# Kernel tuning notes

Measured on AMD Instinct MI355X. Metric: run time of the kernel, lower is better.

Reference implementation:

```python
import jax
import jax.numpy as jnp
import numpy as np

EPSILON = 0.05
MAX_STEPS = 50
N0 = 2048
M0 = 2048


def setup_inputs() -> dict:
    key = jax.random.key(0)
    C = jax.random.uniform(key, (N0, M0), dtype=jnp.float32)
    return {"C": C}


def _sinkhorn(C):
    n0, m0 = C.shape
    # dummy=True: pad right by n0 cols, bottom by m0 rows with zeros -> square (n0+m0, m0+n0)
    C = jnp.pad(C, ((0, m0), (0, n0)), mode="constant", constant_values=0.0)
    n, m = C.shape
    logp = jnp.full((n,), -jnp.log(jnp.float32(n)), dtype=C.dtype)
    logq = jnp.full((m,), -jnp.log(jnp.float32(m)), dtype=C.dtype)
    u0 = jnp.zeros((n,), dtype=C.dtype)
    v0 = jnp.zeros((m,), dtype=C.dtype)

    def step(carry, _):
        u, v = carry
        # row update
        log_pi = (u[:, None] + v[None, :] - C) / EPSILON  # (n, m)
        u = u + EPSILON * (logp - jax.scipy.special.logsumexp(log_pi, axis=1))
        # column update (recompute log_pi with new u)
        log_pi = (u[:, None] + v[None, :] - C) / EPSILON
        v = v + EPSILON * (logq - jax.scipy.special.logsumexp(log_pi, axis=0))
        return (u, v), None

    (u, v), _ = jax.lax.scan(step, (u0, v0), None, length=MAX_STEPS)
    log_pi = (u[:, None] + v[None, :] - C) / EPSILON
    log_pi = jnp.minimum(log_pi, 0.0)
    # scale=True
    return jnp.float32(n) * jnp.exp(log_pi)


def reference(C):
    return _sinkhorn(C)
```

## Files before the change

### kernel.cpp

```cpp
#include <hip/hip_runtime.h>


#define INV_N (1.0 / 4096.0)

#define OFF_K 0UL
#define OFF_KT 16777216UL
#define OFF_W 67059712UL
#define OFF_Z 67076096UL
#define OFF_SCAL 67092480UL
#define OFF_SWB 67092544UL
#define OFF_SZB 67094592UL

static __device__ __forceinline__ double fexp(double x) {
  double t = x * 1.4426950408889634074;
  double n = rint(t);
  double r = fma(n, -0.69314718055994530942, x);
  double p = 2.7557319223985890653e-7;
  p = fma(p, r, 2.7557319223985890653e-6);
  p = fma(p, r, 2.4801587301587301587e-5);
  p = fma(p, r, 1.9841269841269841270e-4);
  p = fma(p, r, 1.3888888888888888889e-3);
  p = fma(p, r, 8.3333333333333333333e-3);
  p = fma(p, r, 4.1666666666666666667e-2);
  p = fma(p, r, 1.6666666666666666667e-1);
  p = fma(p, r, 0.5);
  p = fma(p, r, 1.0);
  p = fma(p, r, 1.0);
  long long bits = ((long long)(1023 + (int)n)) << 52;
  return p * __longlong_as_double(bits);
}

__global__ __launch_bounds__(256) void k_build(const float* __restrict__ C, char* base) {
  float* K = (float*)(base + OFF_K);
  float* KT = (float*)(base + OFF_KT);
  __shared__ float s_t[64][65];
  int b = blockIdx.x, tid = threadIdx.x;
  int ti = b >> 5, tj = b & 31;
  int r0 = tid >> 6, c = tid & 63;
#pragma unroll
  for (int k = 0; k < 16; ++k) {
    int r = r0 + 4 * k;
    int row = ti * 64 + r, col = tj * 64 + c;
    float f = (float)fexp(-20.0 * (double)C[(size_t)row * 2048 + col]);
    K[(size_t)row * 2048 + col] = f;
    s_t[r][c] = f;
  }
  __syncthreads();
#pragma unroll
  for (int k = 0; k < 16; ++k) {
    int r = r0 + 4 * k;
    KT[(size_t)(tj * 64 + r) * 2048 + ti * 64 + c] = s_t[c][r];
  }
  if (b == 0) {
    double* z = (double*)(base + OFF_Z);
    double* scal = (double*)(base + OFF_SCAL);
    double* SzB = (double*)(base + OFF_SZB);
    for (int t = tid; t < 2048; t += 256) z[t] = 1.0;
    SzB[tid] = (tid == 0) ? 2048.0 : 0.0;
    if (tid == 0) scal[1] = 1.0;
  }
}

__global__ __launch_bounds__(512) void k_half(const float* __restrict__ M,
                                              const double* __restrict__ vin,
                                              double* __restrict__ vout,
                                              const double* __restrict__ SpIn,
                                              double* __restrict__ SpOut,
                                              const double* __restrict__ padIn,
                                              double* __restrict__ padOut) {
  __shared__ double s_z[2048];
  __shared__ double s_w[8];
  int tid = threadIdx.x, b = blockIdx.x;
  const double2* zg = (const double2*)vin;
  ((double2*)s_z)[tid] = zg[tid];
  ((double2*)s_z)[tid + 512] = zg[tid + 512];
  double pads = *padIn;
  __syncthreads();
  int wv = tid >> 6, l = tid & 63;
  int i = b * 8 + wv;
  const float4* Mr = (const float4*)(M + (size_t)i * 2048);
  const double2* zr = (const double2*)s_z;
  double a0 = 0, a1 = 0, a2 = 0, a3 = 0;
#pragma unroll
  for (int k = 0; k < 8; ++k) {
    float4 m = Mr[l + 64 * k];
    double2 z0 = zr[2 * (l + 64 * k)];
    double2 z1 = zr[2 * (l + 64 * k) + 1];
    a0 = fma((double)m.x, z0.x, a0);
    a1 = fma((double)m.y, z0.y, a1);
    a2 = fma((double)m.z, z1.x, a2);
    a3 = fma((double)m.w, z1.y, a3);
  }
  double acc = (a0 + a1) + (a2 + a3);
#pragma unroll
  for (int off = 32; off; off >>= 1) acc += __shfl_xor(acc, off, 64);
  double wi = INV_N / (acc + 2048.0 * pads);
  if (l == 0) {
    vout[i] = wi;
    s_w[wv] = wi;
  }
  __syncthreads();
  if (tid == 0) {
    double s = 0;
#pragma unroll
    for (int q = 0; q < 8; ++q) s += s_w[q];
    SpOut[b] = s;
  }
  if (b == 0 && wv == 7) {
    double t = SpIn[l] + SpIn[l + 64] + SpIn[l + 128] + SpIn[l + 192];
#pragma unroll
    for (int off = 32; off; off >>= 1) t += __shfl_xor(t, off, 64);
    if (l == 0) *padOut = INV_N / (t + 2048.0 * pads);
  }
}

__global__ __launch_bounds__(512) void k_out_top(const float* __restrict__ C, char* base) {
  const double* w = (const double*)(base + OFF_W);
  const double* z = (const double*)(base + OFF_Z);
  const double* scal = (const double*)(base + OFF_SCAL);
  float* out = (float*)base;
  __shared__ double s_z[2048];
  __shared__ double s_w[8];
  int tid = threadIdx.x, b = blockIdx.x;
  const double2* zg = (const double2*)z;
  ((double2*)s_z)[tid] = zg[tid];
  ((double2*)s_z)[tid + 512] = zg[tid + 512];
  if (tid < 8) s_w[tid] = w[b * 8 + tid];
  double zpad = scal[1];
  __syncthreads();
  int wv = tid >> 6, l = tid & 63;
  int i = b * 8 + wv;
  double wi = s_w[wv];
  const float4* Cr = (const float4*)(C + (size_t)i * 2048);
  const double2* zr = (const double2*)s_z;
  float* orow = out + (size_t)i * 4096;
#pragma unroll 2
  for (int k = 0; k < 8; ++k) {
    float4 cv = Cr[l + 64 * k];
    double2 z0 = zr[2 * (l + 64 * k)];
    double2 z1 = zr[2 * (l + 64 * k) + 1];
    float4 f;
    f.x = (float)(4096.0 * fmin(wi * z0.x * fexp(-20.0 * (double)cv.x), 1.0));
    f.y = (float)(4096.0 * fmin(wi * z0.y * fexp(-20.0 * (double)cv.y), 1.0));
    f.z = (float)(4096.0 * fmin(wi * z1.x * fexp(-20.0 * (double)cv.z), 1.0));
    f.w = (float)(4096.0 * fmin(wi * z1.y * fexp(-20.0 * (double)cv.w), 1.0));
    ((float4*)orow)[l + 64 * k] = f;
  }
  float cr = (float)(4096.0 * fmin(wi * zpad, 1.0));
  float4 fc;
  fc.x = cr; fc.y = cr; fc.z = cr; fc.w = cr;
#pragma unroll
  for (int k = 0; k < 8; ++k) ((float4*)(orow + 2048))[l + 64 * k] = fc;
}

__global__ __launch_bounds__(512) void k_out_bot(char* base) {
  const double* z = (const double*)(base + OFF_Z);
  const double* scal = (const double*)(base + OFF_SCAL);
  float* out = (float*)base;
  __shared__ float s_val[2048];
  int tid = threadIdx.x, b = blockIdx.x;
  double wpad = scal[0], zpad = scal[1];
  {
    int j = tid * 4;
    double2 z0 = ((const double2*)(z + j))[0];
    double2 z1 = ((const double2*)(z + j))[1];
    s_val[j + 0] = (float)(4096.0 * fmin(wpad * z0.x, 1.0));
    s_val[j + 1] = (float)(4096.0 * fmin(wpad * z0.y, 1.0));
    s_val[j + 2] = (float)(4096.0 * fmin(wpad * z1.x, 1.0));
    s_val[j + 3] = (float)(4096.0 * fmin(wpad * z1.y, 1.0));
  }
  float cf = (float)(4096.0 * fmin(wpad * zpad, 1.0));
  __syncthreads();
  int wv = tid >> 6, l = tid & 63;
  int row = 2048 + b * 8 + wv;
  if (row <= 4092) {
    float4* orow = (float4*)(out + (size_t)row * 4096);
    float4 fc;
    fc.x = cf; fc.y = cf; fc.z = cf; fc.w = cf;
#pragma unroll
    for (int k = 0; k < 8; ++k) orow[l + 64 * k] = ((const float4*)s_val)[l + 64 * k];
#pragma unroll
    for (int k = 0; k < 8; ++k) orow[512 + l + 64 * k] = fc;
  }
}

__global__ __launch_bounds__(512) void k_out_tail(char* base) {
  const double* z = (const double*)(base + OFF_Z);
  const double* scal = (const double*)(base + OFF_SCAL);
  float* out = (float*)base;
  __shared__ float s_val[2048];
  int tid = threadIdx.x;
  double wpad = scal[0], zpad = scal[1];
  {
    int j = tid * 4;
    double2 z0 = ((const double2*)(z + j))[0];
    double2 z1 = ((const double2*)(z + j))[1];
    s_val[j + 0] = (float)(4096.0 * fmin(wpad * z0.x, 1.0));
    s_val[j + 1] = (float)(4096.0 * fmin(wpad * z0.y, 1.0));
    s_val[j + 2] = (float)(4096.0 * fmin(wpad * z1.x, 1.0));
    s_val[j + 3] = (float)(4096.0 * fmin(wpad * z1.y, 1.0));
  }
  float cf = (float)(4096.0 * fmin(wpad * zpad, 1.0));
  __syncthreads();
  float4 fc;
  fc.x = cf; fc.y = cf; fc.z = cf; fc.w = cf;
  for (int row = 4093; row <= 4095; ++row) {
    float4* orow = (float4*)(out + (size_t)row * 4096);
    for (int t = tid; t < 1024; t += 512)
      orow[t] = (t < 512) ? ((const float4*)s_val)[t] : fc;
  }
}

extern "C" void kernel_launch(void* const* d_in, const int* in_sizes, int n_in,
                              void* d_out, int out_size, void* d_ws, size_t ws_size,
                              hipStream_t stream) {
  (void)in_sizes; (void)n_in; (void)d_ws; (void)ws_size; (void)out_size;
  const float* C = (const float*)d_in[0];
  char* base = (char*)d_out;
  const float* K = (const float*)(base + OFF_K);
  const float* KT = (const float*)(base + OFF_KT);
  double* w = (double*)(base + OFF_W);
  double* z = (double*)(base + OFF_Z);
  double* scal = (double*)(base + OFF_SCAL);
  double* SwB = (double*)(base + OFF_SWB);
  double* SzB = (double*)(base + OFF_SZB);

  k_build<<<1024, 256, 0, stream>>>(C, base);
  for (int t = 0; t < 50; ++t) {
    k_half<<<256, 512, 0, stream>>>(K, z, w, SzB, SwB, scal + 1, scal + 0);
    k_half<<<256, 512, 0, stream>>>(KT, w, z, SwB, SzB, scal + 0, scal + 1);
  }
  k_out_top<<<256, 512, 0, stream>>>(C, base);
  k_out_bot<<<256, 512, 0, stream>>>(base);
  k_out_tail<<<1, 512, 0, stream>>>(base);
}
```

Before: 468.0 us.

## Fuse Sinkhorn iterations into one persistent kernel with register-resident K and grid barriers

Replaces the 100 per-half-step kernel launches and the three output kernels with a single persistent kernel of 128 blocks. Each block keeps its two rows of K and K^T in registers for all iterations and synchronises the grid through an atomic-counter barrier. This removes launch overhead and the repeated re-streaming of the kernel matrices from memory every half step. In exchange it relies on all 128 blocks being co-resident to avoid deadlock, carries heavy register pressure (64 float2 per thread), and uses a spin-wait barrier.

```diff
diff --git a/kernel.cpp b/kernel.cpp
--- a/kernel.cpp
+++ b/kernel.cpp
@@ -2,14 +2,15 @@
 
 
 #define INV_N (1.0 / 4096.0)
-
-#define OFF_K 0UL
-#define OFF_KT 16777216UL
+#define NBLK 128u
+
+#define OFF_KT 0UL
 #define OFF_W 67059712UL
 #define OFF_Z 67076096UL
 #define OFF_SCAL 67092480UL
 #define OFF_SWB 67092544UL
 #define OFF_SZB 67094592UL
+#define OFF_CNT 67096640UL
 
 static __device__ __forceinline__ double fexp(double x) {
   double t = x * 1.4426950408889634074;
@@ -31,7 +32,6 @@
 }
 
 __global__ __launch_bounds__(256) void k_build(const float* __restrict__ C, char* base) {
-  float* K = (float*)(base + OFF_K);
   float* KT = (float*)(base + OFF_KT);
   __shared__ float s_t[64][65];
   int b = blockIdx.x, tid = threadIdx.x;
@@ -41,9 +41,7 @@
   for (int k = 0; k < 16; ++k) {
     int r = r0 + 4 * k;
     int row = ti * 64 + r, col = tj * 64 + c;
-    float f = (float)fexp(-20.0 * (double)C[(size_t)row * 2048 + col]);
-    K[(size_t)row * 2048 + col] = f;
-    s_t[r][c] = f;
+    s_t[r][c] = (float)fexp(-20.0 * (double)C[(size_t)row * 2048 + col]);
   }
   __syncthreads();
 #pragma unroll
@@ -55,159 +53,161 @@
     double* z = (double*)(base + OFF_Z);
     double* scal = (double*)(base + OFF_SCAL);
     double* SzB = (double*)(base + OFF_SZB);
+    unsigned* cnt = (unsigned*)(base + OFF_CNT);
     for (int t = tid; t < 2048; t += 256) z[t] = 1.0;
-    SzB[tid] = (tid == 0) ? 2048.0 : 0.0;
-    if (tid == 0) scal[1] = 1.0;
-  }
-}
-
-__global__ __launch_bounds__(512) void k_half(const float* __restrict__ M,
-                                              const double* __restrict__ vin,
-                                              double* __restrict__ vout,
-                                              const double* __restrict__ SpIn,
-                                              double* __restrict__ SpOut,
-                                              const double* __restrict__ padIn,
-                                              double* __restrict__ padOut) {
-  __shared__ double s_z[2048];
-  __shared__ double s_w[8];
-  int tid = threadIdx.x, b = blockIdx.x;
-  const double2* zg = (const double2*)vin;
-  ((double2*)s_z)[tid] = zg[tid];
-  ((double2*)s_z)[tid + 512] = zg[tid + 512];
-  double pads = *padIn;
-  __syncthreads();
-  int wv = tid >> 6, l = tid & 63;
-  int i = b * 8 + wv;
-  const float4* Mr = (const float4*)(M + (size_t)i * 2048);
-  const double2* zr = (const double2*)s_z;
-  double a0 = 0, a1 = 0, a2 = 0, a3 = 0;
-#pragma unroll
-  for (int k = 0; k < 8; ++k) {
-    float4 m = Mr[l + 64 * k];
-    double2 z0 = zr[2 * (l + 64 * k)];
-    double2 z1 = zr[2 * (l + 64 * k) + 1];
-    a0 = fma((double)m.x, z0.x, a0);
-    a1 = fma((double)m.y, z0.y, a1);
-    a2 = fma((double)m.z, z1.x, a2);
-    a3 = fma((double)m.w, z1.y, a3);
-  }
-  double acc = (a0 + a1) + (a2 + a3);
-#pragma unroll
-  for (int off = 32; off; off >>= 1) acc += __shfl_xor(acc, off, 64);
-  double wi = INV_N / (acc + 2048.0 * pads);
+    if (tid < 128) SzB[tid] = (tid == 0) ? 2048.0 : 0.0;
+    if (tid == 0) { scal[1] = 1.0; *cnt = 0u; }
+  }
+}
+
+static __device__ __forceinline__ void gsync(unsigned* cnt, unsigned target) {
+  __syncthreads();
+  if (threadIdx.x == 0) {
+    __threadfence();
+    __hip_atomic_fetch_add(cnt, 1u, __ATOMIC_RELAXED, __HIP_MEMORY_SCOPE_AGENT);
+    while (__hip_atomic_load(cnt, __ATOMIC_RELAXED, __HIP_MEMORY_SCOPE_AGENT) < target)
+      __builtin_amdgcn_s_sleep(2);
+    __threadfence();
+  }
+  __syncthreads();
+  asm volatile("" ::: "memory");
+}
+
+static __device__ __forceinline__ void half_phase(
+    const float2 (&ka)[16], const float2 (&kb)[16], const double* __restrict__ vin,
+    double* __restrict__ vout, const double* __restrict__ SpIn, double* __restrict__ SpOut,
+    const double* padIn, double* padOut, double* s_v, double* s_w16,
+    int tid, int b, int wv, int l, int i0, int i1) {
+  const double2* vg = (const double2*)vin;
+  ((double2*)s_v)[tid] = vg[tid];
+  ((double2*)s_v)[tid + 512] = vg[tid + 512];
+  double pads = __hip_atomic_load((double*)padIn, __ATOMIC_RELAXED, __HIP_MEMORY_SCOPE_AGENT);
+  __syncthreads();
+  const double2* vz = (const double2*)s_v;
+  double a0 = 0, a1 = 0, b0 = 0, b1 = 0;
+#pragma unroll
+  for (int k = 0; k < 16; ++k) {
+    double2 p = vz[l + 64 * k];
+    a0 = fma((double)ka[k].x, p.x, a0);
+    a1 = fma((double)ka[k].y, p.y, a1);
+    b0 = fma((double)kb[k].x, p.x, b0);
+    b1 = fma((double)kb[k].y, p.y, b1);
+  }
+  double accA = a0 + a1, accB = b0 + b1;
+#pragma unroll
+  for (int off = 32; off; off >>= 1) {
+    accA += __shfl_xor(accA, off, 64);
+    accB += __shfl_xor(accB, off, 64);
+  }
+  double wiA = INV_N / (accA + 2048.0 * pads);
+  double wiB = INV_N / (accB + 2048.0 * pads);
   if (l == 0) {
-    vout[i] = wi;
-    s_w[wv] = wi;
+    vout[i0] = wiA; s_w16[wv] = wiA;
+    vout[i1] = wiB; s_w16[8 + wv] = wiB;
+  }
+  if (b == 0 && wv == 7) {
+    double tp = SpIn[l] + SpIn[l + 64];
+#pragma unroll
+    for (int off = 32; off; off >>= 1) tp += __shfl_xor(tp, off, 64);
+    if (l == 0) *padOut = INV_N / (tp + 2048.0 * pads);
   }
   __syncthreads();
   if (tid == 0) {
     double s = 0;
 #pragma unroll
-    for (int q = 0; q < 8; ++q) s += s_w[q];
+    for (int q = 0; q < 16; ++q) s += s_w16[q];
     SpOut[b] = s;
   }
-  if (b == 0 && wv == 7) {
-    double t = SpIn[l] + SpIn[l + 64] + SpIn[l + 128] + SpIn[l + 192];
-#pragma unroll
-    for (int off = 32; off; off >>= 1) t += __shfl_xor(t, off, 64);
-    if (l == 0) *padOut = INV_N / (t + 2048.0 * pads);
-  }
-}
-
-__global__ __launch_bounds__(512) void k_out_top(const float* __restrict__ C, char* base) {
-  const double* w = (const double*)(base + OFF_W);
-  const double* z = (const double*)(base + OFF_Z);
-  const double* scal = (const double*)(base + OFF_SCAL);
+}
+
+__global__ __launch_bounds__(512, 2) void k_loop(const float* __restrict__ C, char* base) {
+  double* w = (double*)(base + OFF_W);
+  double* z = (double*)(base + OFF_Z);
+  double* scal = (double*)(base + OFF_SCAL);
+  double* SwB = (double*)(base + OFF_SWB);
+  double* SzB = (double*)(base + OFF_SZB);
+  unsigned* cnt = (unsigned*)(base + OFF_CNT);
+  const float* KT = (const float*)(base + OFF_KT);
   float* out = (float*)base;
-  __shared__ double s_z[2048];
-  __shared__ double s_w[8];
-  int tid = threadIdx.x, b = blockIdx.x;
-  const double2* zg = (const double2*)z;
-  ((double2*)s_z)[tid] = zg[tid];
-  ((double2*)s_z)[tid + 512] = zg[tid + 512];
-  if (tid < 8) s_w[tid] = w[b * 8 + tid];
-  double zpad = scal[1];
-  __syncthreads();
-  int wv = tid >> 6, l = tid & 63;
-  int i = b * 8 + wv;
-  double wi = s_w[wv];
-  const float4* Cr = (const float4*)(C + (size_t)i * 2048);
-  const double2* zr = (const double2*)s_z;
-  float* orow = out + (size_t)i * 4096;
-#pragma unroll 2
-  for (int k = 0; k < 8; ++k) {
-    float4 cv = Cr[l + 64 * k];
-    double2 z0 = zr[2 * (l + 64 * k)];
-    double2 z1 = zr[2 * (l + 64 * k) + 1];
-    float4 f;
-    f.x = (float)(4096.0 * fmin(wi * z0.x * fexp(-20.0 * (double)cv.x), 1.0));
-    f.y = (float)(4096.0 * fmin(wi * z0.y * fexp(-20.0 * (double)cv.y), 1.0));
-    f.z = (float)(4096.0 * fmin(wi * z1.x * fexp(-20.0 * (double)cv.z), 1.0));
-    f.w = (float)(4096.0 * fmin(wi * z1.y * fexp(-20.0 * (double)cv.w), 1.0));
-    ((float4*)orow)[l + 64 * k] = f;
-  }
-  float cr = (float)(4096.0 * fmin(wi * zpad, 1.0));
-  float4 fc;
-  fc.x = cr; fc.y = cr; fc.z = cr; fc.w = cr;
-#pragma unroll
-  for (int k = 0; k < 8; ++k) ((float4*)(orow + 2048))[l + 64 * k] = fc;
-}
-
-__global__ __launch_bounds__(512) void k_out_bot(char* base) {
-  const double* z = (const double*)(base + OFF_Z);
-  const double* scal = (const double*)(base + OFF_SCAL);
-  float* out = (float*)base;
-  __shared__ float s_val[2048];
-  int tid = threadIdx.x, b = blockIdx.x;
-  double wpad = scal[0], zpad = scal[1];
+
+  __shared__ double s_v[2048];
+  __shared__ float s_valf[2048];
+  __shared__ double s_w16[16];
+
+  const int tid = threadIdx.x, b = blockIdx.x;
+  const int wv = tid >> 6, l = tid & 63;
+  const int i0 = b * 16 + wv, i1 = i0 + 8;
+
+  float2 kra[16], krb[16], kca[16], kcb[16];
   {
-    int j = tid * 4;
-    double2 z0 = ((const double2*)(z + j))[0];
-    double2 z1 = ((const double2*)(z + j))[1];
-    s_val[j + 0] = (float)(4096.0 * fmin(wpad * z0.x, 1.0));
-    s_val[j + 1] = (float)(4096.0 * fmin(wpad * z0.y, 1.0));
-    s_val[j + 2] = (float)(4096.0 * fmin(wpad * z1.x, 1.0));
-    s_val[j + 3] = (float)(4096.0 * fmin(wpad * z1.y, 1.0));
-  }
-  float cf = (float)(4096.0 * fmin(wpad * zpad, 1.0));
-  __syncthreads();
-  int wv = tid >> 6, l = tid & 63;
-  int row = 2048 + b * 8 + wv;
-  if (row <= 4092) {
-    float4* orow = (float4*)(out + (size_t)row * 4096);
-    float4 fc;
-    fc.x = cf; fc.y = cf; fc.z = cf; fc.w = cf;
-#pragma unroll
-    for (int k = 0; k < 8; ++k) orow[l + 64 * k] = ((const float4*)s_val)[l + 64 * k];
-#pragma unroll
-    for (int k = 0; k < 8; ++k) orow[512 + l + 64 * k] = fc;
-  }
-}
-
-__global__ __launch_bounds__(512) void k_out_tail(char* base) {
-  const double* z = (const double*)(base + OFF_Z);
-  const double* scal = (const double*)(base + OFF_SCAL);
-  float* out = (float*)base;
-  __shared__ float s_val[2048];
-  int tid = threadIdx.x;
-  double wpad = scal[0], zpad = scal[1];
+    const float2* cA = (const float2*)(C + (size_t)i0 * 2048);
+    const float2* cB = (const float2*)(C + (size_t)i1 * 2048);
+    const float2* tA = (const float2*)(KT + (size_t)i0 * 2048);
+    const float2* tB = (const float2*)(KT + (size_t)i1 * 2048);
+#pragma unroll
+    for (int k = 0; k < 16; ++k) {
+      float2 ca = cA[l + 64 * k], cb = cB[l + 64 * k];
+      kra[k].x = (float)fexp(-20.0 * (double)ca.x);
+      kra[k].y = (float)fexp(-20.0 * (double)ca.y);
+      krb[k].x = (float)fexp(-20.0 * (double)cb.x);
+      krb[k].y = (float)fexp(-20.0 * (double)cb.y);
+      kca[k] = tA[l + 64 * k];
+      kcb[k] = tB[l + 64 * k];
+    }
+  }
+
+  unsigned bar = 0;
+  for (int t = 0; t < 50; ++t) {
+    half_phase(kra, krb, z, w, SzB, SwB, scal + 1, scal + 0, s_v, s_w16, tid, b, wv, l, i0, i1);
+    ++bar; gsync(cnt, NBLK * bar);
+    half_phase(kca, kcb, w, z, SwB, SzB, scal + 0, scal + 1, s_v, s_w16, tid, b, wv, l, i0, i1);
+    ++bar; gsync(cnt, NBLK * bar);
+  }
+
   {
-    int j = tid * 4;
-    double2 z0 = ((const double2*)(z + j))[0];
-    double2 z1 = ((const double2*)(z + j))[1];
-    s_val[j + 0] = (float)(4096.0 * fmin(wpad * z0.x, 1.0));
-    s_val[j + 1] = (float)(4096.0 * fmin(wpad * z0.y, 1.0));
-    s_val[j + 2] = (float)(4096.0 * fmin(wpad * z1.x, 1.0));
-    s_val[j + 3] = (float)(4096.0 * fmin(wpad * z1.y, 1.0));
-  }
-  float cf = (float)(4096.0 * fmin(wpad * zpad, 1.0));
-  __syncthreads();
-  float4 fc;
-  fc.x = cf; fc.y = cf; fc.z = cf; fc.w = cf;
-  for (int row = 4093; row <= 4095; ++row) {
-    float4* orow = (float4*)(out + (size_t)row * 4096);
-    for (int t = tid; t < 1024; t += 512)
-      orow[t] = (t < 512) ? ((const float4*)s_val)[t] : fc;
+    const double2* zg = (const double2*)z;
+    double2 z0 = zg[tid], z1 = zg[tid + 512];
+    ((double2*)s_v)[tid] = z0;
+    ((double2*)s_v)[tid + 512] = z1;
+    double wpad = __hip_atomic_load(&scal[0], __ATOMIC_RELAXED, __HIP_MEMORY_SCOPE_AGENT);
+    double zpad = __hip_atomic_load(&scal[1], __ATOMIC_RELAXED, __HIP_MEMORY_SCOPE_AGENT);
+    if (tid < 16) s_w16[tid] = w[b * 16 + tid];
+    s_valf[2 * tid] = (float)(4096.0 * fmin(wpad * z0.x, 1.0));
+    s_valf[2 * tid + 1] = (float)(4096.0 * fmin(wpad * z0.y, 1.0));
+    s_valf[1024 + 2 * tid] = (float)(4096.0 * fmin(wpad * z1.x, 1.0));
+    s_valf[1024 + 2 * tid + 1] = (float)(4096.0 * fmin(wpad * z1.y, 1.0));
+    ++bar; gsync(cnt, NBLK * bar);
+
+    const double2* vz = (const double2*)s_v;
+    float cf = (float)(4096.0 * fmin(wpad * zpad, 1.0));
+    float4 fcb; fcb.x = cf; fcb.y = cf; fcb.z = cf; fcb.w = cf;
+
+#pragma unroll
+    for (int rr = 0; rr < 2; ++rr) {
+      const int i = rr ? i1 : i0;
+      double wi = s_w16[rr ? (8 + wv) : wv];
+      const float2* crow = (const float2*)(C + (size_t)i * 2048);
+      float2* orow2 = (float2*)(out + (size_t)i * 4096);
+#pragma unroll 4
+      for (int k = 0; k < 16; ++k) {
+        float2 cv = crow[l + 64 * k];
+        double2 p = vz[l + 64 * k];
+        float2 f;
+        f.x = (float)(4096.0 * fmin(wi * p.x * fexp(-20.0 * (double)cv.x), 1.0));
+        f.y = (float)(4096.0 * fmin(wi * p.y * fexp(-20.0 * (double)cv.y), 1.0));
+        orow2[l + 64 * k] = f;
+      }
+      float cr = (float)(4096.0 * fmin(wi * zpad, 1.0));
+      float4 fct; fct.x = cr; fct.y = cr; fct.z = cr; fct.w = cr;
+      float* orow = out + (size_t)i * 4096;
+#pragma unroll
+      for (int k = 0; k < 8; ++k) ((float4*)(orow + 2048))[l + 64 * k] = fct;
+      float* brow = out + (size_t)(2048 + i) * 4096;
+#pragma unroll
+      for (int k = 0; k < 8; ++k) ((float4*)brow)[l + 64 * k] = ((const float4*)s_valf)[l + 64 * k];
+#pragma unroll
+      for (int k = 0; k < 8; ++k) ((float4*)(brow + 2048))[l + 64 * k] = fcb;
+    }
   }
 }
 
@@ -217,20 +217,6 @@
   (void)in_sizes; (void)n_in; (void)d_ws; (void)ws_size; (void)out_size;
   const float* C = (const float*)d_in[0];
   char* base = (char*)d_out;
-  const float* K = (const float*)(base + OFF_K);
-  const float* KT = (const float*)(base + OFF_KT);
-  double* w = (double*)(base + OFF_W);
-  double* z = (double*)(base + OFF_Z);
-  double* scal = (double*)(base + OFF_SCAL);
-  double* SwB = (double*)(base + OFF_SWB);
-  double* SzB = (double*)(base + OFF_SZB);
-
   k_build<<<1024, 256, 0, stream>>>(C, base);
-  for (int t = 0; t < 50; ++t) {
-    k_half<<<256, 512, 0, stream>>>(K, z, w, SzB, SwB, scal + 1, scal + 0);
-    k_half<<<256, 512, 0, stream>>>(KT, w, z, SwB, SzB, scal + 0, scal + 1);
-  }
-  k_out_top<<<256, 512, 0, stream>>>(C, base);
-  k_out_bot<<<256, 512, 0, stream>>>(base);
-  k_out_tail<<<1, 512, 0, stream>>>(base);
-}
+  k_loop<<<128, 512, 0, stream>>>(C, base);
+}
```

Measured after the change: 1.181 ms. +152.4%, slower.

## Fuse row and column Sinkhorn half-steps into one kernel using atomic column sums

Applied to the files above, without the earlier changes.

Removes the transposed copy of K and the separate column-update kernel. Each iteration is now a single kernel. It computes row scalings from K, then immediately accumulates the K^T·w column sums from the same rows via double-precision atomics into a rotating triple buffer. The next iteration derives z from those sums. This halves the number of launches and the K reads per iteration, at the cost of contended atomics and a nondeterministic summation order.

```diff
diff --git a/kernel.cpp b/kernel.cpp
--- a/kernel.cpp
+++ b/kernel.cpp
@@ -4,12 +4,10 @@
 #define INV_N (1.0 / 4096.0)
 
 #define OFF_K 0UL
-#define OFF_KT 16777216UL
-#define OFF_W 67059712UL
-#define OFF_Z 67076096UL
-#define OFF_SCAL 67092480UL
-#define OFF_SWB 67092544UL
-#define OFF_SZB 67094592UL
+#define OFF_ACC (4090UL * 16384UL)
+#define OFF_W (4093UL * 16384UL)
+#define OFF_P (4094UL * 16384UL)
+#define OFF_WS (OFF_P + 512UL)
 
 static __device__ __forceinline__ double fexp(double x) {
   double t = x * 1.4426950408889634074;
@@ -32,105 +30,129 @@
 
 __global__ __launch_bounds__(256) void k_build(const float* __restrict__ C, char* base) {
   float* K = (float*)(base + OFF_K);
-  float* KT = (float*)(base + OFF_KT);
-  __shared__ float s_t[64][65];
-  int b = blockIdx.x, tid = threadIdx.x;
-  int ti = b >> 5, tj = b & 31;
-  int r0 = tid >> 6, c = tid & 63;
-#pragma unroll
-  for (int k = 0; k < 16; ++k) {
-    int r = r0 + 4 * k;
-    int row = ti * 64 + r, col = tj * 64 + c;
-    float f = (float)fexp(-20.0 * (double)C[(size_t)row * 2048 + col]);
-    K[(size_t)row * 2048 + col] = f;
-    s_t[r][c] = f;
-  }
-  __syncthreads();
-#pragma unroll
-  for (int k = 0; k < 16; ++k) {
-    int r = r0 + 4 * k;
-    KT[(size_t)(tj * 64 + r) * 2048 + ti * 64 + c] = s_t[c][r];
-  }
-  if (b == 0) {
-    double* z = (double*)(base + OFF_Z);
-    double* scal = (double*)(base + OFF_SCAL);
-    double* SzB = (double*)(base + OFF_SZB);
-    for (int t = tid; t < 2048; t += 256) z[t] = 1.0;
-    SzB[tid] = (tid == 0) ? 2048.0 : 0.0;
-    if (tid == 0) scal[1] = 1.0;
-  }
-}
-
-__global__ __launch_bounds__(512) void k_half(const float* __restrict__ M,
-                                              const double* __restrict__ vin,
-                                              double* __restrict__ vout,
-                                              const double* __restrict__ SpIn,
-                                              double* __restrict__ SpOut,
-                                              const double* __restrict__ padIn,
-                                              double* __restrict__ padOut) {
+  int gid = blockIdx.x * 256 + threadIdx.x;
+#pragma unroll
+  for (int q = 0; q < 4; ++q) {
+    int idx = gid + q * 262144;
+    float4 c = ((const float4*)C)[idx];
+    float4 f;
+    f.x = (float)fexp(-20.0 * (double)c.x);
+    f.y = (float)fexp(-20.0 * (double)c.y);
+    f.z = (float)fexp(-20.0 * (double)c.z);
+    f.w = (float)fexp(-20.0 * (double)c.w);
+    ((float4*)K)[idx] = f;
+  }
+  if (blockIdx.x == 0) {
+    double* A1 = (double*)(base + OFF_ACC) + 2048;
+    for (int q = threadIdx.x; q < 2048; q += 256) A1[q] = 0.0;
+    double* ws = (double*)(base + OFF_WS);
+    if (threadIdx.x < 51) ws[threadIdx.x] = 0.0;
+  }
+}
+
+__global__ __launch_bounds__(512) void k_iter(char* base, int t) {
+  const float* K = (const float*)(base + OFF_K);
+  double* ACC = (double*)(base + OFF_ACC);
+  double* W = (double*)(base + OFF_W);
+  double* Pa = (double*)(base + OFF_P);
+  double* WS = (double*)(base + OFF_WS);
+
   __shared__ double s_z[2048];
   __shared__ double s_w[8];
-  int tid = threadIdx.x, b = blockIdx.x;
-  const double2* zg = (const double2*)vin;
-  ((double2*)s_z)[tid] = zg[tid];
-  ((double2*)s_z)[tid + 512] = zg[tid + 512];
-  double pads = *padIn;
-  __syncthreads();
-  int wv = tid >> 6, l = tid & 63;
-  int i = b * 8 + wv;
-  const float4* Mr = (const float4*)(M + (size_t)i * 2048);
+
+  const int tid = threadIdx.x, b = blockIdx.x;
+  const int wv = tid >> 6, l = tid & 63;
+  const int i = b * 8 + wv;
+
+  double P0;
+  if (t == 0) {
+    P0 = 1.0;
+    s_z[tid] = 1.0; s_z[tid + 512] = 1.0; s_z[tid + 1024] = 1.0; s_z[tid + 1536] = 1.0;
+  } else {
+    const double Pm1 = Pa[t];
+    P0 = INV_N / (WS[t] + 2048.0 * Pm1);
+    const double* Ain = ACC + (size_t)(t % 3) * 2048;
+    const double c = 2048.0 * Pm1;
+    s_z[tid] = INV_N / (Ain[tid] + c);
+    s_z[tid + 512] = INV_N / (Ain[tid + 512] + c);
+    s_z[tid + 1024] = INV_N / (Ain[tid + 1024] + c);
+    s_z[tid + 1536] = INV_N / (Ain[tid + 1536] + c);
+  }
+  if (tid < 8) (ACC + (size_t)((t + 2) % 3) * 2048)[b * 8 + tid] = 0.0;
+  __syncthreads();
+
+  const float4* Kr = (const float4*)(K + (size_t)i * 2048);
   const double2* zr = (const double2*)s_z;
-  double a0 = 0, a1 = 0, a2 = 0, a3 = 0;
+  double a0 = 0, a1 = 0, a2 = 0, a3 = 0, ts = 0;
 #pragma unroll
   for (int k = 0; k < 8; ++k) {
-    float4 m = Mr[l + 64 * k];
+    float4 m = Kr[l + 64 * k];
     double2 z0 = zr[2 * (l + 64 * k)];
     double2 z1 = zr[2 * (l + 64 * k) + 1];
     a0 = fma((double)m.x, z0.x, a0);
     a1 = fma((double)m.y, z0.y, a1);
     a2 = fma((double)m.z, z1.x, a2);
     a3 = fma((double)m.w, z1.y, a3);
+    ts += (z0.x + z0.y) + (z1.x + z1.y);
   }
   double acc = (a0 + a1) + (a2 + a3);
 #pragma unroll
-  for (int off = 32; off; off >>= 1) acc += __shfl_xor(acc, off, 64);
-  double wi = INV_N / (acc + 2048.0 * pads);
+  for (int off = 32; off; off >>= 1) {
+    acc += __shfl_xor(acc, off, 64);
+    ts += __shfl_xor(ts, off, 64);
+  }
+  double wi = INV_N / (acc + 2048.0 * P0);
+  double P1 = INV_N / (ts + 2048.0 * P0);
   if (l == 0) {
-    vout[i] = wi;
     s_w[wv] = wi;
-  }
-  __syncthreads();
+    W[i] = wi;
+  }
+  if (b == 0 && tid == 0) Pa[t + 1] = P1;
+  __syncthreads();
+
+  double* Aout = ACC + (size_t)((t + 1) % 3) * 2048;
+  const int jb = (((wv + b) & 7) << 8) + 4 * l;
+  double p0 = 0, p1 = 0, p2 = 0, p3 = 0;
+#pragma unroll
+  for (int r = 0; r < 8; ++r) {
+    float4 kv = *(const float4*)(K + (size_t)(b * 8 + r) * 2048 + jb);
+    double wr = s_w[r];
+    p0 = fma(wr, (double)kv.x, p0);
+    p1 = fma(wr, (double)kv.y, p1);
+    p2 = fma(wr, (double)kv.z, p2);
+    p3 = fma(wr, (double)kv.w, p3);
+  }
+  unsafeAtomicAdd(Aout + jb + 0, p0);
+  unsafeAtomicAdd(Aout + jb + 1, p1);
+  unsafeAtomicAdd(Aout + jb + 2, p2);
+  unsafeAtomicAdd(Aout + jb + 3, p3);
   if (tid == 0) {
-    double s = 0;
-#pragma unroll
-    for (int q = 0; q < 8; ++q) s += s_w[q];
-    SpOut[b] = s;
-  }
-  if (b == 0 && wv == 7) {
-    double t = SpIn[l] + SpIn[l + 64] + SpIn[l + 128] + SpIn[l + 192];
-#pragma unroll
-    for (int off = 32; off; off >>= 1) t += __shfl_xor(t, off, 64);
-    if (l == 0) *padOut = INV_N / (t + 2048.0 * pads);
+    double s = ((s_w[0] + s_w[1]) + (s_w[2] + s_w[3])) + ((s_w[4] + s_w[5]) + (s_w[6] + s_w[7]));
+    unsafeAtomicAdd(WS + t + 1, s);
   }
 }
 
 __global__ __launch_bounds__(512) void k_out_top(const float* __restrict__ C, char* base) {
-  const double* w = (const double*)(base + OFF_W);
-  const double* z = (const double*)(base + OFF_Z);
-  const double* scal = (const double*)(base + OFF_SCAL);
+  const double* A2 = (const double*)(base + OFF_ACC) + 2 * 2048;
+  const double* W = (const double*)(base + OFF_W);
+  const double* Pa = (const double*)(base + OFF_P);
+  const double* WS = (const double*)(base + OFF_WS);
   float* out = (float*)base;
   __shared__ double s_z[2048];
-  __shared__ double s_w[8];
+  __shared__ double s_w8[8];
   int tid = threadIdx.x, b = blockIdx.x;
-  const double2* zg = (const double2*)z;
-  ((double2*)s_z)[tid] = zg[tid];
-  ((double2*)s_z)[tid + 512] = zg[tid + 512];
-  if (tid < 8) s_w[tid] = w[b * 8 + tid];
-  double zpad = scal[1];
+  double wpad = Pa[50];
+  double zpad = INV_N / (WS[50] + 2048.0 * wpad);
+  const double c = 2048.0 * wpad;
+  s_z[tid] = INV_N / (A2[tid] + c);
+  s_z[tid + 512] = INV_N / (A2[tid + 512] + c);
+  s_z[tid + 1024] = INV_N / (A2[tid + 1024] + c);
+  s_z[tid + 1536] = INV_N / (A2[tid + 1536] + c);
+  if (tid < 8) s_w8[tid] = W[b * 8 + tid];
   __syncthreads();
   int wv = tid >> 6, l = tid & 63;
   int i = b * 8 + wv;
-  double wi = s_w[wv];
+  double wi = s_w8[wv];
   const float4* Cr = (const float4*)(C + (size_t)i * 2048);
   const double2* zr = (const double2*)s_z;
   float* orow = out + (size_t)i * 4096;
@@ -147,89 +169,71 @@
     ((float4*)orow)[l + 64 * k] = f;
   }
   float cr = (float)(4096.0 * fmin(wi * zpad, 1.0));
-  float4 fc;
-  fc.x = cr; fc.y = cr; fc.z = cr; fc.w = cr;
-#pragma unroll
-  for (int k = 0; k < 8; ++k) ((float4*)(orow + 2048))[l + 64 * k] = fc;
+  float4 fct; fct.x = cr; fct.y = cr; fct.z = cr; fct.w = cr;
+#pragma unroll
+  for (int k = 0; k < 8; ++k) ((float4*)(orow + 2048))[l + 64 * k] = fct;
 }
 
 __global__ __launch_bounds__(512) void k_out_bot(char* base) {
-  const double* z = (const double*)(base + OFF_Z);
-  const double* scal = (const double*)(base + OFF_SCAL);
+  const double* A2 = (const double*)(base + OFF_ACC) + 2 * 2048;
+  const double* Pa = (const double*)(base + OFF_P);
+  const double* WS = (const double*)(base + OFF_WS);
   float* out = (float*)base;
   __shared__ float s_val[2048];
   int tid = threadIdx.x, b = blockIdx.x;
-  double wpad = scal[0], zpad = scal[1];
-  {
-    int j = tid * 4;
-    double2 z0 = ((const double2*)(z + j))[0];
-    double2 z1 = ((const double2*)(z + j))[1];
-    s_val[j + 0] = (float)(4096.0 * fmin(wpad * z0.x, 1.0));
-    s_val[j + 1] = (float)(4096.0 * fmin(wpad * z0.y, 1.0));
-    s_val[j + 2] = (float)(4096.0 * fmin(wpad * z1.x, 1.0));
-    s_val[j + 3] = (float)(4096.0 * fmin(wpad * z1.y, 1.0));
-  }
+  double wpad = Pa[50];
+  double zpad = INV_N / (WS[50] + 2048.0 * wpad);
+  const double c = 2048.0 * wpad;
+  s_val[tid] = (float)(4096.0 * fmin(wpad * (INV_N / (A2[tid] + c)), 1.0));
+  s_val[tid + 512] = (float)(4096.0 * fmin(wpad * (INV_N / (A2[tid + 512] + c)), 1.0));
+  s_val[tid + 1024] = (float)(4096.0 * fmin(wpad * (INV_N / (A2[tid + 1024] + c)), 1.0));
+  s_val[tid + 1536] = (float)(4096.0 * fmin(wpad * (INV_N / (A2[tid + 1536] + c)), 1.0));
   float cf = (float)(4096.0 * fmin(wpad * zpad, 1.0));
   __syncthreads();
   int wv = tid >> 6, l = tid & 63;
   int row = 2048 + b * 8 + wv;
-  if (row <= 4092) {
-    float4* orow = (float4*)(out + (size_t)row * 4096);
-    float4 fc;
-    fc.x = cf; fc.y = cf; fc.z = cf; fc.w = cf;
-#pragma unroll
-    for (int k = 0; k < 8; ++k) orow[l + 64 * k] = ((const float4*)s_val)[l + 64 * k];
-#pragma unroll
-    for (int k = 0; k < 8; ++k) orow[512 + l + 64 * k] = fc;
+  if (row <= 4089) {
+    float* orow = out + (size_t)row * 4096;
+    float4 fc; fc.x = cf; fc.y = cf; fc.z = cf; fc.w = cf;
+#pragma unroll
+    for (int k = 0; k < 8; ++k) ((float4*)orow)[l + 64 * k] = ((const float4*)s_val)[l + 64 * k];
+#pragma unroll
+    for (int k = 0; k < 8; ++k) ((float4*)(orow + 2048))[l + 64 * k] = fc;
   }
 }
 
 __global__ __launch_bounds__(512) void k_out_tail(char* base) {
-  const double* z = (const double*)(base + OFF_Z);
-  const double* scal = (const double*)(base + OFF_SCAL);
+  const double* A2 = (const double*)(base + OFF_ACC) + 2 * 2048;
+  const double* Pa = (const double*)(base + OFF_P);
+  const double* WS = (const double*)(base + OFF_WS);
   float* out = (float*)base;
   __shared__ float s_val[2048];
   int tid = threadIdx.x;
-  double wpad = scal[0], zpad = scal[1];
-  {
-    int j = tid * 4;
-    double2 z0 = ((const double2*)(z + j))[0];
-    double2 z1 = ((const double2*)(z + j))[1];
-    s_val[j + 0] = (float)(4096.0 * fmin(wpad * z0.x, 1.0));
-    s_val[j + 1] = (float)(4096.0 * fmin(wpad * z0.y, 1.0));
-    s_val[j + 2] = (float)(4096.0 * fmin(wpad * z1.x, 1.0));
-    s_val[j + 3] = (float)(4096.0 * fmin(wpad * z1.y, 1.0));
-  }
+  double wpad = Pa[50];
+  double zpad = INV_N / (WS[50] + 2048.0 * wpad);
+  const double c = 2048.0 * wpad;
+  s_val[tid] = (float)(4096.0 * fmin(wpad * (INV_N / (A2[tid] + c)), 1.0));
+  s_val[tid + 512] = (float)(4096.0 * fmin(wpad * (INV_N / (A2[tid + 512] + c)), 1.0));
+  s_val[tid + 1024] = (float)(4096.0 * fmin(wpad * (INV_N / (A2[tid + 1024] + c)), 1.0));
+  s_val[tid + 1536] = (float)(4096.0 * fmin(wpad * (INV_N / (A2[tid + 1536] + c)), 1.0));
   float cf = (float)(4096.0 * fmin(wpad * zpad, 1.0));
   __syncthreads();
-  float4 fc;
-  fc.x = cf; fc.y = cf; fc.z = cf; fc.w = cf;
-  for (int row = 4093; row <= 4095; ++row) {
+  float4 fc; fc.x = cf; fc.y = cf; fc.z = cf; fc.w = cf;
+  for (int row = 4090; row <= 4095; ++row) {
     float4* orow = (float4*)(out + (size_t)row * 4096);
-    for (int t = tid; t < 1024; t += 512)
-      orow[t] = (t < 512) ? ((const float4*)s_val)[t] : fc;
+    for (int q = tid; q < 1024; q += 512)
+      orow[q] = (q < 512) ? ((const float4*)s_val)[q] : fc;
   }
 }
 
 extern "C" void kernel_launch(void* const* d_in, const int* in_sizes, int n_in,
                               void* d_out, int out_size, void* d_ws, size_t ws_size,
                               hipStream_t stream) {
-  (void)in_sizes; (void)n_in; (void)d_ws; (void)ws_size; (void)out_size;
+  (void)in_sizes; (void)n_in; (void)out_size; (void)d_ws; (void)ws_size;
   const float* C = (const float*)d_in[0];
   char* base = (char*)d_out;
-  const float* K = (const float*)(base + OFF_K);
-  const float* KT = (const float*)(base + OFF_KT);
-  double* w = (double*)(base + OFF_W);
-  double* z = (double*)(base + OFF_Z);
-  double* scal = (double*)(base + OFF_SCAL);
-  double* SwB = (double*)(base + OFF_SWB);
-  double* SzB = (double*)(base + OFF_SZB);
-
   k_build<<<1024, 256, 0, stream>>>(C, base);
-  for (int t = 0; t < 50; ++t) {
-    k_half<<<256, 512, 0, stream>>>(K, z, w, SzB, SwB, scal + 1, scal + 0);
-    k_half<<<256, 512, 0, stream>>>(KT, w, z, SwB, SzB, scal + 0, scal + 1);
-  }
+  for (int t = 0; t < 50; ++t) k_iter<<<256, 512, 0, stream>>>(base, t);
   k_out_top<<<256, 512, 0, stream>>>(C, base);
   k_out_bot<<<256, 512, 0, stream>>>(base);
   k_out_tail<<<1, 512, 0, stream>>>(base);
```

Measured after the change: 1.497 ms. 3.2x slower.
